# Kernel tuning notes

Measured on AMD Instinct MI355X. Metric: run time of the kernel, lower is better.

Reference implementation:

```python
import jax, jax.numpy as jnp
import numpy as np

B, S, D, H, EXPAND = 4, 2048, 256, 4, 4
DH = D // H
EPS = 1e-3  # keras BatchNormalization default epsilon
NEG = -1e9  # keras Softmax masking constant


def setup_inputs() -> dict:
    key = jax.random.key(0)
    ks = jax.random.split(key, 8)
    x = jax.random.normal(ks[0], (B, S, D), dtype=jnp.float32)
    mask = jax.random.randint(ks[1], (B, S), 0, 2) > 0
    mask = mask.at[:, 0].set(True)  # ensure each row has a valid token
    sc = 1.0 / np.sqrt(D)
    return {
        "x": x,
        "mask": mask,
        "bn1_gamma": jnp.ones((D,), jnp.float32),
        "bn1_beta": jnp.zeros((D,), jnp.float32),
        "bn1_mean": jax.random.normal(ks[2], (D,), jnp.float32) * 0.1,
        "bn1_var": jnp.ones((D,), jnp.float32),
        "qkv_w": jax.random.normal(ks[3], (D, 3 * D), jnp.float32) * sc,
        "proj_w": jax.random.normal(ks[4], (D, D), jnp.float32) * sc,
        "bn2_gamma": jnp.ones((D,), jnp.float32),
        "bn2_beta": jnp.zeros((D,), jnp.float32),
        "bn2_mean": jax.random.normal(ks[5], (D,), jnp.float32) * 0.1,
        "bn2_var": jnp.ones((D,), jnp.float32),
        "w1": jax.random.normal(ks[6], (D, EXPAND * D), jnp.float32) * sc,
        "w2": jax.random.normal(ks[7], (EXPAND * D, D), jnp.float32) * (sc / 2.0),
    }


def _bn(x, gamma, beta, mean, var):
    # inference-mode BatchNormalization over the channel axis
    return (x - mean) * jax.lax.rsqrt(var + EPS) * gamma + beta


def reference(x, mask, bn1_gamma, bn1_beta, bn1_mean, bn1_var, qkv_w, proj_w,
              bn2_gamma, bn2_beta, bn2_mean, bn2_var, w1, w2):
    scale = D ** (-0.5)
    # --- attention sub-block ---
    skip = x
    h = _bn(x, bn1_gamma, bn1_beta, bn1_mean, bn1_var)
    qkv = h @ qkv_w                                    # [B,S,3D]
    qkv = qkv.reshape(B, S, H, 3 * DH).transpose(0, 2, 1, 3)  # [B,H,S,3dh]
    q, k, v = qkv[..., :DH], qkv[..., DH:2 * DH], qkv[..., 2 * DH:]
    scores = jnp.einsum('bhqd,bhkd->bhqk', q, k) * scale      # [B,H,S,S]
    scores = scores + jnp.where(mask[:, None, None, :], 0.0, NEG)
    attn = jax.nn.softmax(scores, axis=-1)
    o = jnp.einsum('bhqk,bhkd->bhqd', attn, v)                # [B,H,S,dh]
    o = o.transpose(0, 2, 1, 3).reshape(B, S, D) @ proj_w
    x = o + skip
    # --- FFN sub-block ---
    skip = x
    h = _bn(x, bn2_gamma, bn2_beta, bn2_mean, bn2_var)
    h = jax.nn.swish(h @ w1)                                  # [B,S,4D]
    h = h @ w2
    return h + skip
```

## Files before the change

### kernel.cpp

```cpp
#include <hip/hip_runtime.h>
#include <math.h>

#define S_ 2048
#define D_ 256
#define B_ 4
#define H_ 4

typedef __attribute__((ext_vector_type(8))) short  bh8;
typedef __attribute__((ext_vector_type(4))) float  fx4;
typedef __attribute__((ext_vector_type(4))) unsigned short us4;
typedef __attribute__((ext_vector_type(4))) unsigned int   ux4;

__device__ inline unsigned short bf16r(float f) {
    unsigned int u = __builtin_bit_cast(unsigned int, f);
    return (unsigned short)((u + 0x7FFFu + ((u >> 16) & 1u)) >> 16);
}
__device__ inline unsigned int cvtpk(float a, float b) {
    unsigned int r;
    asm("v_cvt_pk_bf16_f32 %0, %1, %2" : "=v"(r) : "v"(a), "v"(b));
    return r;
}
__device__ inline float vexp2(float x) {
    float r;
    asm volatile("v_exp_f32 %0, %1\n\ts_nop 1" : "=v"(r) : "v"(x));
    return r;
}

__device__ inline size_t fragoff(int m, int k, int K32) {
    return ((size_t)(m >> 4) * K32 + (k >> 5)) * 512
         + (size_t)((((k >> 3) & 3) * 16 + (m & 15)) * 8 + (k & 7));
}

__global__ __launch_bounds__(256) void prep_all_k(
    const float* __restrict__ qkv_w, const float* __restrict__ proj_w,
    const float* __restrict__ w1,    const float* __restrict__ w2,
    unsigned short* __restrict__ qkv_wt, unsigned short* __restrict__ proj_wt,
    unsigned short* __restrict__ w1t,    unsigned short* __restrict__ w2t,
    const float* __restrict__ x,
    const float* __restrict__ g1, const float* __restrict__ b1,
    const float* __restrict__ m1, const float* __restrict__ v1,
    unsigned short* __restrict__ xb,
    const int* __restrict__ mask, float* __restrict__ maskf)
{
    const int bidx = blockIdx.x;
    if (bidx < 768) {
        const float* W; unsigned short* Wt; int K, N, u0;
        if (bidx < 192)      { W = qkv_w;  Wt = qkv_wt;  K = 256;  N = 768;  u0 = bidx * 256; }
        else if (bidx < 256) { W = proj_w; Wt = proj_wt; K = 256;  N = 256;  u0 = (bidx - 192) * 256; }
        else if (bidx < 512) { W = w1;     Wt = w1t;     K = 256;  N = 1024; u0 = (bidx - 256) * 256; }
        else                 { W = w2;     Wt = w2t;     K = 1024; N = 256;  u0 = (bidx - 512) * 256; }
        const int u = u0 + threadIdx.x;
        const int k4 = u / N, n = u % N;
        us4 tv;
        #pragma unroll
        for (int j = 0; j < 4; ++j) tv[j] = bf16r(W[(size_t)(k4 * 4 + j) * N + n]);
        *(us4*)&Wt[fragoff(n, k4 * 4, K >> 5)] = tv;
    } else if (bidx < 2816) {
        const int i = (bidx - 768) * 256 + threadIdx.x;
        const int m = i >> 6, c0 = (i & 63) * 4;
        float4 xv = *(const float4*)&x[(size_t)i * 4];
        float vv[4] = {xv.x, xv.y, xv.z, xv.w};
        us4 tv;
        #pragma unroll
        for (int j = 0; j < 4; ++j) {
            int c = c0 + j;
            float s = g1[c] * rsqrtf(v1[c] + 1e-3f);
            tv[j] = bf16r(vv[j] * s + (b1[c] - m1[c] * s));
        }
        *(us4*)&xb[fragoff(m, c0, 8)] = tv;
    } else {
        const int i = (bidx - 2816) * 256 + threadIdx.x;
        maskf[i] = mask[i] ? 0.0f : -1e9f;
    }
}

template<int E>
__global__ __launch_bounds__(64) void gemm_frag_k(
    const unsigned short* __restrict__ Af, const unsigned short* __restrict__ Bf,
    int N, int K,
    const float* __restrict__ res, float* __restrict__ outf,
    unsigned short* __restrict__ outb, unsigned short* __restrict__ kf_o,
    unsigned short* __restrict__ vf_o,
    const float* __restrict__ g2, const float* __restrict__ b2,
    const float* __restrict__ m2, const float* __restrict__ v2)
{
    const int l = threadIdx.x;
    const int qi = l & 15, g = l >> 4;
    const int nt0 = blockIdx.x * 4, mt0 = blockIdx.y * 4;
    const int K32 = K >> 5;

    fx4 acc[4][4];
    #pragma unroll
    for (int mi = 0; mi < 4; ++mi)
        #pragma unroll
        for (int ni = 0; ni < 4; ++ni) acc[mi][ni] = (fx4){0.f, 0.f, 0.f, 0.f};

    const unsigned short* Ab = Af + (size_t)mt0 * K32 * 512 + l * 8;
    const unsigned short* Bb = Bf + (size_t)nt0 * K32 * 512 + l * 8;

    #pragma unroll 2
    for (int kt = 0; kt < K32; ++kt) {
        bh8 af[4], bf[4];
        #pragma unroll
        for (int mi = 0; mi < 4; ++mi)
            af[mi] = *(const bh8*)(Ab + ((size_t)mi * K32 + kt) * 512);
        #pragma unroll
        for (int ni = 0; ni < 4; ++ni)
            bf[ni] = *(const bh8*)(Bb + ((size_t)ni * K32 + kt) * 512);
        #pragma unroll
        for (int mi = 0; mi < 4; ++mi)
            #pragma unroll
            for (int ni = 0; ni < 4; ++ni)
                acc[mi][ni] = __builtin_amdgcn_mfma_f32_16x16x32_bf16(
                    af[mi], bf[ni], acc[mi][ni], 0, 0, 0);
    }

    #pragma unroll
    for (int ni = 0; ni < 4; ++ni) {
        const int nf = (nt0 + ni) * 16;
        if (E == 0) {
            const int h = nf / 192, rem = nf % 192;
            const int region = rem / 64;
            const int c = rem % 64 + qi;
            #pragma unroll
            for (int mi = 0; mi < 4; ++mi) {
                #pragma unroll
                for (int r = 0; r < 4; ++r) {
                    const int m = (mt0 + mi) * 16 + g * 4 + r;
                    const int s = m & 2047;
                    const size_t bh = (size_t)((m >> 11) * 4 + h);
                    float a = acc[mi][ni][r];
                    if (region < 2) {
                        size_t off = (((bh * 128 + (s >> 4)) * 2 + (c >> 5)) * 64
                                      + ((c >> 3) & 3) * 16 + (s & 15)) * 8 + (c & 7);
                        if (region == 0)
                            outb[off] = bf16r(a * (0.0625f * 1.44269504f));
                        else
                            kf_o[off] = bf16r(a);
                    } else {
                        size_t off = ((((bh * 32 + (s >> 6)) * 4 + (c >> 4)) * 2
                                      + ((s >> 5) & 1)) * 64
                                      + ((s >> 3) & 3) * 16 + (c & 15)) * 8 + (s & 7);
                        vf_o[off] = bf16r(a);
                    }
                }
            }
        } else if (E == 1) {
            const int n = nf + qi;
            const float s2 = g2[n] * rsqrtf(v2[n] + 1e-3f);
            const float o2 = b2[n] - m2[n] * s2;
            #pragma unroll
            for (int mi = 0; mi < 4; ++mi) {
                #pragma unroll
                for (int r = 0; r < 4; ++r) {
                    const int m = (mt0 + mi) * 16 + g * 4 + r;
                    const size_t idx = (size_t)m * N + n;
                    float rv = acc[mi][ni][r] + res[idx];
                    outf[idx] = rv;
                    outb[fragoff(m, n, 8)] = bf16r(rv * s2 + o2);
                }
            }
        } else if (E == 2) {
            const int n = nf + qi;
            #pragma unroll
            for (int mi = 0; mi < 4; ++mi) {
                #pragma unroll
                for (int r = 0; r < 4; ++r) {
                    const int m = (mt0 + mi) * 16 + g * 4 + r;
                    float a = acc[mi][ni][r];
                    outb[fragoff(m, n, 32)] = bf16r(a / (1.0f + __expf(-a)));
                }
            }
        } else {
            const int n = nf + qi;
            #pragma unroll
            for (int mi = 0; mi < 4; ++mi) {
                #pragma unroll
                for (int r = 0; r < 4; ++r) {
                    const int m = (mt0 + mi) * 16 + g * 4 + r;
                    const size_t idx = (size_t)m * N + n;
                    outf[idx] = acc[mi][ni][r] + res[idx];
                }
            }
        }
    }
}

__global__ __launch_bounds__(256) void attn_mfma_k(
    const unsigned short* __restrict__ qf,
    const unsigned short* __restrict__ kf,
    const unsigned short* __restrict__ vf,
    const float* __restrict__ maskf,
    unsigned short* __restrict__ ob)
{
    __shared__ fx4  Ol[2][64][8];
    __shared__ float Ll[2][64][2];

    const int bid = blockIdx.x;
    const int bh = bid & 15, qt = bid >> 4;
    const int b = bh >> 2, h = bh & 3;
    const int t = threadIdx.x;
    const int w = t >> 6, lane = t & 63;
    const int g = lane >> 4, qi = lane & 15;
    const int qh = w & 1;
    const int khalf = w >> 1;

    bh8 qA0, qA1, qB0, qB1;
    {
        const unsigned short* qp =
            qf + (size_t)(bh * 128 + qt * 4 + qh * 2) * 1024 + lane * 8;
        qA0 = *(const bh8*)(qp);
        qA1 = *(const bh8*)(qp + 512);
        qB0 = *(const bh8*)(qp + 1024);
        qB1 = *(const bh8*)(qp + 1536);
    }

    fx4 oA[4], oB[4];
    #pragma unroll
    for (int dt = 0; dt < 4; ++dt) {
        oA[dt] = (fx4){0.f, 0.f, 0.f, 0.f};
        oB[dt] = (fx4){0.f, 0.f, 0.f, 0.f};
    }
    float lsA = 0.f, lsB = 0.f;

    const unsigned short* kcur = kf + (size_t)bh * 131072 + khalf * 65536 + lane * 8;
    const unsigned short* vcur = vf + (size_t)bh * 131072 + khalf * 65536 + lane * 8;
    const float* mcur = maskf + b * 2048 + khalf * 1024 + g * 4;

    bh8 kfA[4][2], kfB[4][2], afA[4][2], afB[4][2];
    fx4 mvA[4], mvB[4];

#define LOADK(KF, MV) {                                                       \
    KF[0][0] = *(const bh8*)(kcur);        KF[0][1] = *(const bh8*)(kcur + 512);  \
    KF[1][0] = *(const bh8*)(kcur + 1024); KF[1][1] = *(const bh8*)(kcur + 1536); \
    KF[2][0] = *(const bh8*)(kcur + 2048); KF[2][1] = *(const bh8*)(kcur + 2560); \
    KF[3][0] = *(const bh8*)(kcur + 3072); KF[3][1] = *(const bh8*)(kcur + 3584); \
    MV[0] = *(const fx4*)(mcur);      MV[1] = *(const fx4*)(mcur + 16);       \
    MV[2] = *(const fx4*)(mcur + 32); MV[3] = *(const fx4*)(mcur + 48);       \
    kcur += 4096; mcur += 64; }

#define LOADV(AF) {                                                           \
    AF[0][0] = *(const bh8*)(vcur);        AF[0][1] = *(const bh8*)(vcur + 512);  \
    AF[1][0] = *(const bh8*)(vcur + 1024); AF[1][1] = *(const bh8*)(vcur + 1536); \
    AF[2][0] = *(const bh8*)(vcur + 2048); AF[2][1] = *(const bh8*)(vcur + 2560); \
    AF[3][0] = *(const bh8*)(vcur + 3072); AF[3][1] = *(const bh8*)(vcur + 3584); \
    vcur += 4096; }

#define PROCESS(KF, AF, MV) {                                                 \
    fx4 sA[4], sB[4];                                                         \
    _Pragma("unroll")                                                         \
    for (int kt = 0; kt < 4; ++kt) {                                          \
        fx4 zA = MV[kt];                                                      \
        zA = __builtin_amdgcn_mfma_f32_16x16x32_bf16(KF[kt][0], qA0, zA, 0, 0, 0); \
        zA = __builtin_amdgcn_mfma_f32_16x16x32_bf16(KF[kt][1], qA1, zA, 0, 0, 0); \
        sA[kt] = zA;                                                          \
        fx4 zB = MV[kt];                                                      \
        zB = __builtin_amdgcn_mfma_f32_16x16x32_bf16(KF[kt][0], qB0, zB, 0, 0, 0); \
        zB = __builtin_amdgcn_mfma_f32_16x16x32_bf16(KF[kt][1], qB1, zB, 0, 0, 0); \
        sB[kt] = zB;                                                          \
    }                                                                         \
    unsigned int pkA[4][2], pkB[4][2];                                        \
    _Pragma("unroll")                                                         \
    for (int kt = 0; kt < 4; ++kt) {                                          \
        float a0 = vexp2(sA[kt][0]);                                          \
        float a1 = vexp2(sA[kt][1]);                                          \
        float a2 = vexp2(sA[kt][2]);                                          \
        float a3 = vexp2(sA[kt][3]);                                          \
        lsA += (a0 + a1) + (a2 + a3);                                         \
        pkA[kt][0] = cvtpk(a0, a1);                                           \
        pkA[kt][1] = cvtpk(a2, a3);                                           \
        float b0 = vexp2(sB[kt][0]);                                          \
        float b1 = vexp2(sB[kt][1]);                                          \
        float b2 = vexp2(sB[kt][2]);                                          \
        float b3 = vexp2(sB[kt][3]);                                          \
        lsB += (b0 + b1) + (b2 + b3);                                         \
        pkB[kt][0] = cvtpk(b0, b1);                                           \
        pkB[kt][1] = cvtpk(b2, b3);                                           \
    }                                                                         \
    _Pragma("unroll")                                                         \
    for (int c = 0; c < 2; ++c) {                                             \
        unsigned int bwA[4], bwB[4];                                          \
        _Pragma("unroll")                                                     \
        for (int wd = 0; wd < 4; ++wd) {                                      \
            int src = (2 * (g & 1) + (wd >> 1)) * 16 + qi;                    \
            unsigned int vaA = (unsigned int)__shfl((int)pkA[2 * c][wd & 1], src, 64);     \
            unsigned int vbA = (unsigned int)__shfl((int)pkA[2 * c + 1][wd & 1], src, 64); \
            bwA[wd] = (g >= 2) ? vbA : vaA;                                   \
            unsigned int vaB = (unsigned int)__shfl((int)pkB[2 * c][wd & 1], src, 64);     \
            unsigned int vbB = (unsigned int)__shfl((int)pkB[2 * c + 1][wd & 1], src, 64); \
            bwB[wd] = (g >= 2) ? vbB : vaB;                                   \
        }                                                                     \
        bh8 bfA = __builtin_bit_cast(bh8, (ux4){bwA[0], bwA[1], bwA[2], bwA[3]}); \
        bh8 bfB = __builtin_bit_cast(bh8, (ux4){bwB[0], bwB[1], bwB[2], bwB[3]}); \
        _Pragma("unroll")                                                     \
        for (int dt = 0; dt < 4; ++dt) {                                      \
            oA[dt] = __builtin_amdgcn_mfma_f32_16x16x32_bf16(AF[dt][c], bfA, oA[dt], 0, 0, 0); \
            oB[dt] = __builtin_amdgcn_mfma_f32_16x16x32_bf16(AF[dt][c], bfB, oB[dt], 0, 0, 0); \
        }                                                                     \
    } }

    LOADK(kfA, mvA);
    LOADV(afA);
    for (int it = 0; it < 16; it += 2) {
        LOADK(kfB, mvB);
        LOADV(afB);
        PROCESS(kfA, afA, mvA);
        if (it + 2 < 16) {
            LOADK(kfA, mvA);
            LOADV(afA);
        }
        PROCESS(kfB, afB, mvB);
    }
#undef LOADK
#undef LOADV
#undef PROCESS

    const int slot = w & 1;
    if (w >= 2) {
        #pragma unroll
        for (int dt = 0; dt < 4; ++dt) {
            Ol[slot][lane][dt]     = oA[dt];
            Ol[slot][lane][4 + dt] = oB[dt];
        }
        Ll[slot][lane][0] = lsA;
        Ll[slot][lane][1] = lsB;
    }
    __syncthreads();
    if (w < 2) {
        lsA += Ll[slot][lane][0];
        lsB += Ll[slot][lane][1];
        #pragma unroll
        for (int dt = 0; dt < 4; ++dt) {
            fx4 pa = Ol[slot][lane][dt], pb = Ol[slot][lane][4 + dt];
            oA[dt][0] += pa[0]; oA[dt][1] += pa[1]; oA[dt][2] += pa[2]; oA[dt][3] += pa[3];
            oB[dt][0] += pb[0]; oB[dt][1] += pb[1]; oB[dt][2] += pb[2]; oB[dt][3] += pb[3];
        }
        lsA += __shfl_xor(lsA, 16, 64);
        lsA += __shfl_xor(lsA, 32, 64);
        lsB += __shfl_xor(lsB, 16, 64);
        lsB += __shfl_xor(lsB, 32, 64);
        float invA = 1.0f / lsA, invB = 1.0f / lsB;
        const int mA = b * 2048 + qt * 64 + qh * 32 + qi;
        #pragma unroll
        for (int dt = 0; dt < 4; ++dt) {
            us4 ta, tb;
            #pragma unroll
            for (int r = 0; r < 4; ++r) {
                ta[r] = bf16r(oA[dt][r] * invA);
                tb[r] = bf16r(oB[dt][r] * invB);
            }
            const int n0 = h * 64 + dt * 16 + g * 4;
            *(us4*)&ob[fragoff(mA,      n0, 8)] = ta;
            *(us4*)&ob[fragoff(mA + 16, n0, 8)] = tb;
        }
    }
}

extern "C" void kernel_launch(void* const* d_in, const int* in_sizes, int n_in,
                              void* d_out, int out_size, void* d_ws, size_t ws_size,
                              hipStream_t stream) {
    const float* x      = (const float*)d_in[0];
    const int*   mask   = (const int*)  d_in[1];
    const float* bn1_g  = (const float*)d_in[2];
    const float* bn1_b  = (const float*)d_in[3];
    const float* bn1_m  = (const float*)d_in[4];
    const float* bn1_v  = (const float*)d_in[5];
    const float* qkv_w  = (const float*)d_in[6];
    const float* proj_w = (const float*)d_in[7];
    const float* bn2_g  = (const float*)d_in[8];
    const float* bn2_b  = (const float*)d_in[9];
    const float* bn2_m  = (const float*)d_in[10];
    const float* bn2_v  = (const float*)d_in[11];
    const float* w1     = (const float*)d_in[12];
    const float* w2     = (const float*)d_in[13];
    float* out = (float*)d_out;

    char* w8 = (char*)d_ws;
    unsigned short* qkv_wt  = (unsigned short*)(w8 + 0);
    unsigned short* proj_wt = (unsigned short*)(w8 + 393216);
    unsigned short* w1t     = (unsigned short*)(w8 + 524288);
    unsigned short* w2t     = (unsigned short*)(w8 + 1048576);
    float*          maskf   = (float*)         (w8 + 1572864);
    unsigned short* xb      = (unsigned short*)(w8 + 2097152);
    float*          x2      = (float*)         (w8 + 6291456);
    unsigned short* x2nb    = (unsigned short*)(w8 + 14680064);
    unsigned short* qfrag   = (unsigned short*)(w8 + 18874368);
    unsigned short* kfrag   = (unsigned short*)(w8 + 23068672);
    unsigned short* vfrag   = (unsigned short*)(w8 + 27262976);
    unsigned short* ob      = (unsigned short*)(w8 + 31457280);
    unsigned short* h2b     = (unsigned short*)(w8 + 18874368);

    prep_all_k<<<2848, 256, 0, stream>>>(
        qkv_w, proj_w, w1, w2, qkv_wt, proj_wt, w1t, w2t,
        x, bn1_g, bn1_b, bn1_m, bn1_v, xb, mask, maskf);

    gemm_frag_k<0><<<dim3(12, 128), 64, 0, stream>>>(
        xb, qkv_wt, 768, 256, nullptr, nullptr, qfrag, kfrag, vfrag,
        nullptr, nullptr, nullptr, nullptr);

    attn_mfma_k<<<dim3(512), 256, 0, stream>>>(qfrag, kfrag, vfrag, maskf, ob);

    gemm_frag_k<1><<<dim3(4, 128), 64, 0, stream>>>(
        ob, proj_wt, 256, 256, x, x2, x2nb, nullptr, nullptr,
        bn2_g, bn2_b, bn2_m, bn2_v);

    gemm_frag_k<2><<<dim3(16, 128), 64, 0, stream>>>(
        x2nb, w1t, 1024, 256, nullptr, nullptr, h2b, nullptr, nullptr,
        nullptr, nullptr, nullptr, nullptr);

    gemm_frag_k<3><<<dim3(4, 128), 64, 0, stream>>>(
        h2b, w2t, 256, 1024, x2, out, nullptr, nullptr, nullptr,
        nullptr, nullptr, nullptr, nullptr);
}
```

Baseline: 107.7 us.

## Split GEMM K-loop across four waves with shared-memory reduction

Each GEMM block now runs four wavefronts instead of one, and each wave handles a quarter of the K dimension for the same 64x64 output tile. Partial accumulators are written to a 64KB shared buffer, summed after a barrier, and each wave then runs the epilogue for 16 rows. This is meant to cut the serial K-loop latency per block and raise wave-level parallelism on small grids. The cost is LDS traffic, a block barrier, and 64KB of shared memory per block, which limits how many blocks fit on a CU.

```diff
diff --git a/kernel.cpp b/kernel.cpp
--- a/kernel.cpp
+++ b/kernel.cpp
@@ -75,7 +75,7 @@
 }
 
 template<int E>
-__global__ __launch_bounds__(64) void gemm_frag_k(
+__global__ __launch_bounds__(256) void gemm_frag_sk(
     const unsigned short* __restrict__ Af, const unsigned short* __restrict__ Bf,
     int N, int K,
     const float* __restrict__ res, float* __restrict__ outf,
@@ -84,10 +84,11 @@
     const float* __restrict__ g2, const float* __restrict__ b2,
     const float* __restrict__ m2, const float* __restrict__ v2)
 {
-    const int l = threadIdx.x;
+    __shared__ float C4[4][64][64];
+    const int t = threadIdx.x, w = t >> 6, l = t & 63;
     const int qi = l & 15, g = l >> 4;
     const int nt0 = blockIdx.x * 4, mt0 = blockIdx.y * 4;
-    const int K32 = K >> 5;
+    const int K32 = K >> 5, KQ = K32 >> 2;
 
     fx4 acc[4][4];
     #pragma unroll
@@ -95,11 +96,11 @@
         #pragma unroll
         for (int ni = 0; ni < 4; ++ni) acc[mi][ni] = (fx4){0.f, 0.f, 0.f, 0.f};
 
-    const unsigned short* Ab = Af + (size_t)mt0 * K32 * 512 + l * 8;
-    const unsigned short* Bb = Bf + (size_t)nt0 * K32 * 512 + l * 8;
+    const unsigned short* Ab = Af + ((size_t)mt0 * K32 + w * KQ) * 512 + l * 8;
+    const unsigned short* Bb = Bf + ((size_t)nt0 * K32 + w * KQ) * 512 + l * 8;
 
     #pragma unroll 2
-    for (int kt = 0; kt < K32; ++kt) {
+    for (int kt = 0; kt < KQ; ++kt) {
         bh8 af[4], bf[4];
         #pragma unroll
         for (int mi = 0; mi < 4; ++mi)
@@ -114,6 +115,25 @@
                 acc[mi][ni] = __builtin_amdgcn_mfma_f32_16x16x32_bf16(
                     af[mi], bf[ni], acc[mi][ni], 0, 0, 0);
     }
+
+    #pragma unroll
+    for (int mi = 0; mi < 4; ++mi)
+        #pragma unroll
+        for (int ni = 0; ni < 4; ++ni)
+            #pragma unroll
+            for (int r = 0; r < 4; ++r)
+                C4[w][mi * 16 + g * 4 + r][ni * 16 + qi] = acc[mi][ni][r];
+    __syncthreads();
+
+    fx4 o[4];
+    #pragma unroll
+    for (int ni = 0; ni < 4; ++ni)
+        #pragma unroll
+        for (int r = 0; r < 4; ++r) {
+            const int row = w * 16 + g * 4 + r, col = ni * 16 + qi;
+            o[ni][r] = (C4[0][row][col] + C4[1][row][col])
+                     + (C4[2][row][col] + C4[3][row][col]);
+        }
 
     #pragma unroll
     for (int ni = 0; ni < 4; ++ni) {
@@ -123,26 +143,23 @@
             const int region = rem / 64;
             const int c = rem % 64 + qi;
             #pragma unroll
-            for (int mi = 0; mi < 4; ++mi) {
-                #pragma unroll
-                for (int r = 0; r < 4; ++r) {
-                    const int m = (mt0 + mi) * 16 + g * 4 + r;
-                    const int s = m & 2047;
-                    const size_t bh = (size_t)((m >> 11) * 4 + h);
-                    float a = acc[mi][ni][r];
-                    if (region < 2) {
-                        size_t off = (((bh * 128 + (s >> 4)) * 2 + (c >> 5)) * 64
-                                      + ((c >> 3) & 3) * 16 + (s & 15)) * 8 + (c & 7);
-                        if (region == 0)
-                            outb[off] = bf16r(a * (0.0625f * 1.44269504f));
-                        else
-                            kf_o[off] = bf16r(a);
-                    } else {
-                        size_t off = ((((bh * 32 + (s >> 6)) * 4 + (c >> 4)) * 2
-                                      + ((s >> 5) & 1)) * 64
-                                      + ((s >> 3) & 3) * 16 + (c & 15)) * 8 + (s & 7);
-                        vf_o[off] = bf16r(a);
-                    }
+            for (int r = 0; r < 4; ++r) {
+                const int m = (mt0 + w) * 16 + g * 4 + r;
+                const int s = m & 2047;
+                const size_t bh = (size_t)((m >> 11) * 4 + h);
+                float a = o[ni][r];
+                if (region < 2) {
+                    size_t off = (((bh * 128 + (s >> 4)) * 2 + (c >> 5)) * 64
+                                  + ((c >> 3) & 3) * 16 + (s & 15)) * 8 + (c & 7);
+                    if (region == 0)
+                        outb[off] = bf16r(a * (0.0625f * 1.44269504f));
+                    else
+                        kf_o[off] = bf16r(a);
+                } else {
+                    size_t off = ((((bh * 32 + (s >> 6)) * 4 + (c >> 4)) * 2
+                                  + ((s >> 5) & 1)) * 64
+                                  + ((s >> 3) & 3) * 16 + (c & 15)) * 8 + (s & 7);
+                    vf_o[off] = bf16r(a);
                 }
             }
         } else if (E == 1) {
@@ -150,37 +167,28 @@
             const float s2 = g2[n] * rsqrtf(v2[n] + 1e-3f);
             const float o2 = b2[n] - m2[n] * s2;
             #pragma unroll
-            for (int mi = 0; mi < 4; ++mi) {
-                #pragma unroll
-                for (int r = 0; r < 4; ++r) {
-                    const int m = (mt0 + mi) * 16 + g * 4 + r;
-                    const size_t idx = (size_t)m * N + n;
-                    float rv = acc[mi][ni][r] + res[idx];
-                    outf[idx] = rv;
-                    outb[fragoff(m, n, 8)] = bf16r(rv * s2 + o2);
-                }
+            for (int r = 0; r < 4; ++r) {
+                const int m = (mt0 + w) * 16 + g * 4 + r;
+                const size_t idx = (size_t)m * N + n;
+                float rv = o[ni][r] + res[idx];
+                outf[idx] = rv;
+                outb[fragoff(m, n, 8)] = bf16r(rv * s2 + o2);
             }
         } else if (E == 2) {
             const int n = nf + qi;
             #pragma unroll
-            for (int mi = 0; mi < 4; ++mi) {
-                #pragma unroll
-                for (int r = 0; r < 4; ++r) {
-                    const int m = (mt0 + mi) * 16 + g * 4 + r;
-                    float a = acc[mi][ni][r];
-                    outb[fragoff(m, n, 32)] = bf16r(a / (1.0f + __expf(-a)));
-                }
+            for (int r = 0; r < 4; ++r) {
+                const int m = (mt0 + w) * 16 + g * 4 + r;
+                float a = o[ni][r];
+                outb[fragoff(m, n, 32)] = bf16r(a / (1.0f + __expf(-a)));
             }
         } else {
             const int n = nf + qi;
             #pragma unroll
-            for (int mi = 0; mi < 4; ++mi) {
-                #pragma unroll
-                for (int r = 0; r < 4; ++r) {
-                    const int m = (mt0 + mi) * 16 + g * 4 + r;
-                    const size_t idx = (size_t)m * N + n;
-                    outf[idx] = acc[mi][ni][r] + res[idx];
-                }
+            for (int r = 0; r < 4; ++r) {
+                const int m = (mt0 + w) * 16 + g * 4 + r;
+                const size_t idx = (size_t)m * N + n;
+                outf[idx] = o[ni][r] + res[idx];
             }
         }
     }
@@ -394,21 +402,21 @@
         qkv_w, proj_w, w1, w2, qkv_wt, proj_wt, w1t, w2t,
         x, bn1_g, bn1_b, bn1_m, bn1_v, xb, mask, maskf);
 
-    gemm_frag_k<0><<<dim3(12, 128), 64, 0, stream>>>(
+    gemm_frag_sk<0><<<dim3(12, 128), 256, 0, stream>>>(
         xb, qkv_wt, 768, 256, nullptr, nullptr, qfrag, kfrag, vfrag,
         nullptr, nullptr, nullptr, nullptr);
 
     attn_mfma_k<<<dim3(512), 256, 0, stream>>>(qfrag, kfrag, vfrag, maskf, ob);
 
-    gemm_frag_k<1><<<dim3(4, 128), 64, 0, stream>>>(
+    gemm_frag_sk<1><<<dim3(4, 128), 256, 0, stream>>>(
         ob, proj_wt, 256, 256, x, x2, x2nb, nullptr, nullptr,
         bn2_g, bn2_b, bn2_m, bn2_v);
 
-    gemm_frag_k<2><<<dim3(16, 128), 64, 0, stream>>>(
+    gemm_frag_sk<2><<<dim3(16, 128), 256, 0, stream>>>(
         x2nb, w1t, 1024, 256, nullptr, nullptr, h2b, nullptr, nullptr,
         nullptr, nullptr, nullptr, nullptr);
 
-    gemm_frag_k<3><<<dim3(4, 128), 64, 0, stream>>>(
+    gemm_frag_sk<3><<<dim3(4, 128), 256, 0, stream>>>(
         h2b, w2t, 256, 1024, x2, out, nullptr, nullptr, nullptr,
         nullptr, nullptr, nullptr, nullptr);
 }
```

New measurement: 104.0 us. 3.4% less time.
